# Performance work log

Hardware: AMD Instinct MI355X
Metric: run time of the kernel (lower is better)

The kernel has to match this reference:

```python
import jax, jax.numpy as jnp
import numpy as np

NUM_TREE = 64
TREE_DEPTH = 4
NUM_LEAF = 2 ** (TREE_DEPTH + 1)        # 32
NUM_INTERNALS = NUM_LEAF - 1            # 31
IN_DIM = 512
OUT_DIM = 16
BATCH = 8192


def build_route_masks(tree_depth: int, num_internals: int, num_leaf: int) -> np.ndarray:
    """Static gather indices into the [p, 1-p] concatenated prob vector (length 2*num_internals).
    Returns [tree_depth+1, num_leaf]; product over level axis gives leaf path probabilities.
    Mirrors the increment_mask construction in the torch forward."""
    masks = []
    num_repeat = num_leaf // 2
    num_local_internals = 1
    masks.append(np.repeat(np.array([0, num_internals]), num_repeat))
    for _ in range(1, tree_depth + 1):
        num_repeat //= 2
        num_local_internals *= 2
        m = np.repeat(np.arange(num_local_internals - 1, 2 * num_local_internals - 1), 2)
        m = m + np.tile(np.array([0, num_internals]), num_local_internals)
        m = np.repeat(m, num_repeat)
        masks.append(m)
    return np.stack(masks).astype(np.int32)  # [depth+1, num_leaf]


ROUTE_MASKS = jnp.asarray(build_route_masks(TREE_DEPTH, NUM_INTERNALS, NUM_LEAF))


def setup_inputs() -> dict:
    key = jax.random.key(0)
    k1, k2, k3 = jax.random.split(key, 3)
    x = jax.random.normal(k1, (BATCH, IN_DIM), dtype=jnp.float32)
    # xavier-ish scale so sigmoid gates are not saturated
    W = jax.random.normal(k2, (NUM_TREE * NUM_INTERNALS, IN_DIM), dtype=jnp.float32) / np.sqrt(IN_DIM)
    b = jnp.zeros((NUM_TREE * NUM_INTERNALS,), dtype=jnp.float32)
    leafs = jax.random.normal(k3, (NUM_TREE, NUM_LEAF, OUT_DIM), dtype=jnp.float32)
    return {"x": x, "W": W, "b": b, "leafs": leafs}


def reference(x, W, b, leafs) -> jnp.ndarray:
    B = x.shape[0]
    T, L, O = leafs.shape
    I = L - 1
    tree_net = x @ W.T + b                                  # [B, T*I]
    p = jax.nn.sigmoid(tree_net).reshape(B, T, I)           # split per tree
    flat = jnp.concatenate([p, 1.0 - p], axis=-1)           # [B, T, 2I]
    gathered = flat[:, :, ROUTE_MASKS]                      # [B, T, depth+1, L]
    routes = jnp.prod(gathered, axis=2)                     # [B, T, L] leaf path probs
    leafs_sm = jax.nn.softmax(leafs, axis=-1)
    features = routes.reshape(B, T * L)
    out = features @ leafs_sm.reshape(T * L, O) / T
    return out
```

## Files before the change

### kernel.cpp

```cpp
#include <hip/hip_runtime.h>

#define BATCH 8192
#define IN_DIM 512
#define NT 64
#define NI 31
#define NL 32
#define ODIM 16
#define NPAD (NT*NL)

typedef __attribute__((ext_vector_type(8))) short bf16x8;
typedef __attribute__((ext_vector_type(4))) float f32x4;

__device__ __forceinline__ unsigned short f2b(float f) {
  union { float f; unsigned int u; } v; v.f = f;
  unsigned int r = v.u + 0x7fffu + ((v.u >> 16) & 1u);
  return (unsigned short)(r >> 16);
}
__device__ __forceinline__ float b2f(unsigned short h) {
  union { unsigned int u; float f; } v; v.u = ((unsigned int)h) << 16;
  return v.f;
}

__global__ __launch_bounds__(256) void prep_kernel(
    const float* __restrict__ x, const float* __restrict__ W,
    const float* __restrict__ leafs,
    unsigned short* __restrict__ xb, unsigned short* __restrict__ wb,
    float* __restrict__ lsm, float* __restrict__ out)
{
  const int NXg = BATCH * (IN_DIM/8);
  const int NWg = NPAD  * (IN_DIM/8);
  const int NS  = NT*NL;
  const int NZ  = BATCH*ODIM/4;
  int gid = blockIdx.x*256 + threadIdx.x;
  if (gid < NXg) {
    int row = gid >> 6, k8 = gid & 63;
    int kt = k8 >> 2, g = k8 & 3;
    int gs = g ^ ((row >> 1) & 3);
    const float* s = x + (size_t)row*IN_DIM + kt*32 + gs*8;
    float4 v0 = ((const float4*)s)[0], v1 = ((const float4*)s)[1];
    ushort4 o0, o1;
    o0.x=f2b(v0.x); o0.y=f2b(v0.y); o0.z=f2b(v0.z); o0.w=f2b(v0.w);
    o1.x=f2b(v1.x); o1.y=f2b(v1.y); o1.z=f2b(v1.z); o1.w=f2b(v1.w);
    ((ushort4*)xb)[gid*2]   = o0;
    ((ushort4*)xb)[gid*2+1] = o1;
  } else if ((gid -= NXg) < NWg) {
    int row = gid >> 6, k8 = gid & 63;
    int t = row >> 5, i = row & 31;
    int kt = k8 >> 2, g = k8 & 3;
    int gs = g ^ ((row >> 1) & 3);
    ushort4 o0, o1;
    if (i == 31) { o0.x=o0.y=o0.z=o0.w=0; o1=o0; }
    else {
      const float* s = W + (size_t)(t*NI+i)*IN_DIM + kt*32 + gs*8;
      float4 v0 = ((const float4*)s)[0], v1 = ((const float4*)s)[1];
      o0.x=f2b(v0.x); o0.y=f2b(v0.y); o0.z=f2b(v0.z); o0.w=f2b(v0.w);
      o1.x=f2b(v1.x); o1.y=f2b(v1.y); o1.z=f2b(v1.z); o1.w=f2b(v1.w);
    }
    ((ushort4*)wb)[gid*2]   = o0;
    ((ushort4*)wb)[gid*2+1] = o1;
  } else if ((gid -= NWg) < NS) {
    const float* src = leafs + (size_t)gid*ODIM;
    float m = src[0];
    #pragma unroll
    for (int o=1;o<ODIM;++o) m = fmaxf(m, src[o]);
    float e[ODIM]; float s = 0.f;
    #pragma unroll
    for (int o=0;o<ODIM;++o) { e[o] = __expf(src[o]-m); s += e[o]; }
    float inv = 1.f/(s*(float)NT);
    #pragma unroll
    for (int o=0;o<ODIM;++o) lsm[(size_t)gid*ODIM+o] = e[o]*inv;
  } else if ((gid -= NS) < NZ) {
    float4 zero = {0.f,0.f,0.f,0.f};
    ((float4*)out)[gid] = zero;
  }
}

__device__ __forceinline__ void async16(const unsigned short* g, unsigned short* l) {
  __builtin_amdgcn_global_load_lds(
      (const __attribute__((address_space(1))) unsigned int*)g,
      (__attribute__((address_space(3))) unsigned int*)l,
      16, 0, 0);
}

#define STG 12288

__global__ __launch_bounds__(256, 2) void fused_kernel(
    const unsigned short* __restrict__ xb, const unsigned short* __restrict__ wb,
    const float* __restrict__ bias, const float* __restrict__ lsm,
    float* __restrict__ out)
{
  __shared__ __align__(16) unsigned short smem[36864];

  const int tid  = threadIdx.x;
  const int lane = tid & 63;
  const int wave = tid >> 6;
  const int wm = wave & 1, wn = wave >> 1;

  const int bid = blockIdx.x;
  const int m_t = (bid & 7)*4 + (bid >> 7);
  const int n_t = (bid >> 3) & 15;
  const int m0 = m_t * 256, n0 = n_t * 128;

  f32x4 acc[8][4];
  #pragma unroll
  for (int i=0;i<8;++i)
    #pragma unroll
    for (int j=0;j<4;++j) { f32x4 z = {0.f,0.f,0.f,0.f}; acc[i][j] = z; }

  const int srow = lane >> 2, scol = (lane & 3) * 8;
  const unsigned short* gaw = xb + (size_t)(m0 + wave*64 + srow)*IN_DIM + scol;
  const unsigned short* gbw = wb + (size_t)(n0 + wave*32 + srow)*IN_DIM + scol;

  const int l15 = lane & 15, quad = lane >> 4;
  const int cs   = (quad ^ ((l15 >> 1) & 3)) << 3;

  #pragma unroll
  for (int c=0;c<4;++c) async16(gaw + c*16*IN_DIM,      smem + wave*2048 + c*512);
  #pragma unroll
  for (int c=0;c<2;++c) async16(gbw + c*16*IN_DIM,      smem + 8192 + wave*1024 + c*512);
  #pragma unroll
  for (int c=0;c<4;++c) async16(gaw + 32 + c*16*IN_DIM, smem + STG + wave*2048 + c*512);
  #pragma unroll
  for (int c=0;c<2;++c) async16(gbw + 32 + c*16*IN_DIM, smem + STG + 8192 + wave*1024 + c*512);

  unsigned short* st0 = smem;
  unsigned short* st1 = smem + STG;
  unsigned short* st2 = smem + 2*STG;

  for (int kt = 0; kt < 15; ++kt) {
    asm volatile("s_waitcnt vmcnt(6)" ::: "memory");
    __builtin_amdgcn_s_barrier();
    if (kt < 14) {
      const int ko = (kt + 2) * 32;
      #pragma unroll
      for (int c=0;c<4;++c)
        async16(gaw + ko + c*16*IN_DIM, st2 + wave*2048 + c*512);
      #pragma unroll
      for (int c=0;c<2;++c)
        async16(gbw + ko + c*16*IN_DIM, st2 + 8192 + wave*1024 + c*512);
    }
    const unsigned short* As = st0;
    const unsigned short* Bs = st0 + 8192;
    bf16x8 af[8], bfr[4];
    #pragma unroll
    for (int mi=0;mi<8;++mi)
      af[mi] = *(const bf16x8*)(As + (wm*128 + mi*16 + l15)*32 + cs);
    #pragma unroll
    for (int ni=0;ni<4;++ni)
      bfr[ni] = *(const bf16x8*)(Bs + (wn*64 + ni*16 + l15)*32 + cs);
    __builtin_amdgcn_s_setprio(1);
    #pragma unroll
    for (int mi=0;mi<8;++mi)
      #pragma unroll
      for (int ni=0;ni<4;++ni)
        acc[mi][ni] = __builtin_amdgcn_mfma_f32_16x16x32_bf16(
            af[mi], bfr[ni], acc[mi][ni], 0, 0, 0);
    __builtin_amdgcn_s_setprio(0);
    unsigned short* t = st0; st0 = st1; st1 = st2; st2 = t;
  }
  asm volatile("s_waitcnt vmcnt(0)" ::: "memory");
  __builtin_amdgcn_s_barrier();
  {
    const unsigned short* As = st0;
    const unsigned short* Bs = st0 + 8192;
    bf16x8 af[8], bfr[4];
    #pragma unroll
    for (int mi=0;mi<8;++mi)
      af[mi] = *(const bf16x8*)(As + (wm*128 + mi*16 + l15)*32 + cs);
    #pragma unroll
    for (int ni=0;ni<4;++ni)
      bfr[ni] = *(const bf16x8*)(Bs + (wn*64 + ni*16 + l15)*32 + cs);
    __builtin_amdgcn_s_setprio(1);
    #pragma unroll
    for (int mi=0;mi<8;++mi)
      #pragma unroll
      for (int ni=0;ni<4;++ni)
        acc[mi][ni] = __builtin_amdgcn_mfma_f32_16x16x32_bf16(
            af[mi], bfr[ni], acc[mi][ni], 0, 0, 0);
    __builtin_amdgcn_s_setprio(0);
  }

  bf16x8 bleaf[4];
  {
    const int t0 = n_t * 4;
    #pragma unroll
    for (int s=0;s<4;++s) {
      union { bf16x8 v; unsigned short u[8]; } tmp;
      #pragma unroll
      for (int j=0;j<8;++j)
        tmp.u[j] = f2b(lsm[((size_t)(t0+s)*NL + quad*8 + j)*ODIM + l15]);
      bleaf[s] = tmp.v;
    }
  }

  __syncthreads();

  unsigned short* Pt = smem;
  #pragma unroll
  for (int ni=0;ni<4;++ni) {
    int cl = wn*64 + ni*16 + l15;
    int gcol = n0 + cl;
    int tt = gcol >> 5, ii = gcol & 31;
    float bv = (ii < NI) ? bias[tt*NI + ii] : 0.f;
    #pragma unroll
    for (int mi=0;mi<8;++mi) {
      int lrow = wm*128 + mi*16 + quad*4;
      #pragma unroll
      for (int r=0;r<4;++r) {
        float v = acc[mi][ni][r] + bv;
        Pt[(lrow + r)*132 + cl] = f2b(1.f/(1.f + __expf(-v)));
      }
    }
  }
  __syncthreads();

  const int row = tid;
  unsigned int rt[64];
  #pragma unroll
  for (int tl=0; tl<4; ++tl) {
    const short4* pr4 = (const short4*)(Pt + row*132 + tl*32);
    union { short4 v4[8]; unsigned short u[32]; } qb;
    #pragma unroll
    for (int c=0;c<8;++c) qb.v4[c] = pr4[c];
    float q[31];
    #pragma unroll
    for (int i=0;i<31;++i) q[i] = b2f(qb.u[i]);
    float v[32];
    v[0] = q[0]; v[1] = 1.f - q[0];
    #pragma unroll
    for (int d=1; d<=4; ++d) {
      const int s = 1 << d;
      #pragma unroll
      for (int j=s-1; j>=0; --j) {
        float pj = q[(s-1)+j];
        float base = v[j];
        v[2*j]   = base * pj;
        v[2*j+1] = base * (1.f - pj);
      }
    }
    #pragma unroll
    for (int k=0;k<16;++k)
      rt[tl*16+k] = (unsigned int)f2b(v[2*k]) | ((unsigned int)f2b(v[2*k+1]) << 16);
  }
  __syncthreads();

  unsigned int* Rt32 = (unsigned int*)smem;
  {
    uint4* dst = (uint4*)(Rt32 + row*68);
    #pragma unroll
    for (int c=0;c<16;++c) {
      uint4 w; w.x=rt[c*4]; w.y=rt[c*4+1]; w.z=rt[c*4+2]; w.w=rt[c*4+3];
      dst[c] = w;
    }
  }
  __syncthreads();

  const unsigned short* RtS = smem;
  #pragma unroll
  for (int mt=0; mt<4; ++mt) {
    const int mrow = (wave*4 + mt)*16;
    f32x4 a2 = {0.f,0.f,0.f,0.f};
    #pragma unroll
    for (int s=0;s<4;++s) {
      bf16x8 af2 = *(const bf16x8*)(RtS + (mrow + l15)*136 + s*32 + quad*8);
      a2 = __builtin_amdgcn_mfma_f32_16x16x32_bf16(af2, bleaf[s], a2, 0, 0, 0);
    }
    float* op = out + (size_t)(m0 + mrow + quad*4)*ODIM + l15;
    #pragma unroll
    for (int r=0;r<4;++r)
      atomicAdd(op + r*ODIM, a2[r]);
  }
}

extern "C" void kernel_launch(void* const* d_in, const int* in_sizes, int n_in,
                              void* d_out, int out_size, void* d_ws, size_t ws_size,
                              hipStream_t stream) {
  const float* x     = (const float*)d_in[0];
  const float* W     = (const float*)d_in[1];
  const float* b     = (const float*)d_in[2];
  const float* leafs = (const float*)d_in[3];
  float* out = (float*)d_out;

  char* ws = (char*)d_ws;
  unsigned short* xb  = (unsigned short*)ws;
  unsigned short* wb  = (unsigned short*)(ws + 8388608);
  float*          lsm = (float*)(ws + 10485760);

  const int total = BATCH*(IN_DIM/8) + NPAD*(IN_DIM/8) + NT*NL + BATCH*ODIM/4;
  prep_kernel<<<dim3((total + 255)/256), dim3(256), 0, stream>>>(
      x, W, leafs, xb, wb, lsm, out);
  fused_kernel<<<dim3(512), dim3(256), 0, stream>>>(
      xb, wb, b, lsm, out);
}
```

Measured before the change: 104.6 us.

## Fuse x bf16 conversion into GEMM kernel via register-staged loads

Removes the separate pass that converted x to a bf16 workspace. The GEMM kernel now loads fp32 x rows directly into registers, packs them to bf16 with v_cvt_pk_bf16_f32, and writes them swizzled into LDS. The pipeline changes from a 3-stage async ring to double buffering, with register prefetch for A. This drops a full read and write of x in the prep pass but doubles the global bytes the GEMM reads for A. It also adds VALU conversion work and a shallower pipeline inside the main loop.

```diff
diff --git a/kernel.cpp b/kernel.cpp
--- a/kernel.cpp
+++ b/kernel.cpp
@@ -20,30 +20,22 @@
   union { unsigned int u; float f; } v; v.u = ((unsigned int)h) << 16;
   return v.f;
 }
+__device__ __forceinline__ unsigned int cvtpk(float lo, float hi) {
+  unsigned int r;
+  asm("v_cvt_pk_bf16_f32 %0, %1, %2" : "=v"(r) : "v"(lo), "v"(hi));
+  return r;
+}
 
 __global__ __launch_bounds__(256) void prep_kernel(
-    const float* __restrict__ x, const float* __restrict__ W,
-    const float* __restrict__ leafs,
-    unsigned short* __restrict__ xb, unsigned short* __restrict__ wb,
-    float* __restrict__ lsm, float* __restrict__ out)
+    const float* __restrict__ W, const float* __restrict__ leafs,
+    unsigned short* __restrict__ wb, float* __restrict__ lsm,
+    float* __restrict__ out)
 {
-  const int NXg = BATCH * (IN_DIM/8);
-  const int NWg = NPAD  * (IN_DIM/8);
+  const int NWg = NPAD * (IN_DIM/8);
   const int NS  = NT*NL;
   const int NZ  = BATCH*ODIM/4;
   int gid = blockIdx.x*256 + threadIdx.x;
-  if (gid < NXg) {
-    int row = gid >> 6, k8 = gid & 63;
-    int kt = k8 >> 2, g = k8 & 3;
-    int gs = g ^ ((row >> 1) & 3);
-    const float* s = x + (size_t)row*IN_DIM + kt*32 + gs*8;
-    float4 v0 = ((const float4*)s)[0], v1 = ((const float4*)s)[1];
-    ushort4 o0, o1;
-    o0.x=f2b(v0.x); o0.y=f2b(v0.y); o0.z=f2b(v0.z); o0.w=f2b(v0.w);
-    o1.x=f2b(v1.x); o1.y=f2b(v1.y); o1.z=f2b(v1.z); o1.w=f2b(v1.w);
-    ((ushort4*)xb)[gid*2]   = o0;
-    ((ushort4*)xb)[gid*2+1] = o1;
-  } else if ((gid -= NXg) < NWg) {
+  if (gid < NWg) {
     int row = gid >> 6, k8 = gid & 63;
     int t = row >> 5, i = row & 31;
     int kt = k8 >> 2, g = k8 & 3;
@@ -82,14 +74,14 @@
       16, 0, 0);
 }
 
-#define STG 12288
+#define SSTG 12288
 
 __global__ __launch_bounds__(256, 2) void fused_kernel(
-    const unsigned short* __restrict__ xb, const unsigned short* __restrict__ wb,
+    const float* __restrict__ x, const unsigned short* __restrict__ wb,
     const float* __restrict__ bias, const float* __restrict__ lsm,
     float* __restrict__ out)
 {
-  __shared__ __align__(16) unsigned short smem[36864];
+  __shared__ __align__(16) unsigned short smem[34816];
 
   const int tid  = threadIdx.x;
   const int lane = tid & 63;
@@ -108,39 +100,48 @@
     for (int j=0;j<4;++j) { f32x4 z = {0.f,0.f,0.f,0.f}; acc[i][j] = z; }
 
   const int srow = lane >> 2, scol = (lane & 3) * 8;
-  const unsigned short* gaw = xb + (size_t)(m0 + wave*64 + srow)*IN_DIM + scol;
   const unsigned short* gbw = wb + (size_t)(n0 + wave*32 + srow)*IN_DIM + scol;
+
+  const float4* gx4 = (const float4*)(x + (size_t)(m0 + tid)*IN_DIM);
+  const int aswz = (tid >> 1) & 3;
 
   const int l15 = lane & 15, quad = lane >> 4;
   const int cs   = (quad ^ ((l15 >> 1) & 3)) << 3;
 
-  #pragma unroll
-  for (int c=0;c<4;++c) async16(gaw + c*16*IN_DIM,      smem + wave*2048 + c*512);
-  #pragma unroll
-  for (int c=0;c<2;++c) async16(gbw + c*16*IN_DIM,      smem + 8192 + wave*1024 + c*512);
-  #pragma unroll
-  for (int c=0;c<4;++c) async16(gaw + 32 + c*16*IN_DIM, smem + STG + wave*2048 + c*512);
-  #pragma unroll
-  for (int c=0;c<2;++c) async16(gbw + 32 + c*16*IN_DIM, smem + STG + 8192 + wave*1024 + c*512);
-
-  unsigned short* st0 = smem;
-  unsigned short* st1 = smem + STG;
-  unsigned short* st2 = smem + 2*STG;
+  float4 L[8];
+
+  #pragma unroll
+  for (int j=0;j<8;++j) L[j] = gx4[j];
+  {
+    unsigned short* Ad = smem + tid*32;
+    #pragma unroll
+    for (int gsrc=0; gsrc<4; ++gsrc) {
+      uint4 w;
+      w.x = cvtpk(L[2*gsrc].x, L[2*gsrc].y);
+      w.y = cvtpk(L[2*gsrc].z, L[2*gsrc].w);
+      w.z = cvtpk(L[2*gsrc+1].x, L[2*gsrc+1].y);
+      w.w = cvtpk(L[2*gsrc+1].z, L[2*gsrc+1].w);
+      *(uint4*)(Ad + (gsrc ^ aswz)*8) = w;
+    }
+  }
+  #pragma unroll
+  for (int c=0;c<2;++c) async16(gbw + c*16*IN_DIM, smem + 8192 + wave*1024 + c*512);
+  __builtin_amdgcn_sched_barrier(0);
+  #pragma unroll
+  for (int j=0;j<8;++j) L[j] = gx4[8 + j];
 
   for (int kt = 0; kt < 15; ++kt) {
-    asm volatile("s_waitcnt vmcnt(6)" ::: "memory");
+    unsigned short* stc = smem + (kt & 1) * SSTG;
+    unsigned short* stn = smem + ((kt + 1) & 1) * SSTG;
+    asm volatile("s_waitcnt vmcnt(8) lgkmcnt(0)" ::: "memory");
     __builtin_amdgcn_s_barrier();
-    if (kt < 14) {
-      const int ko = (kt + 2) * 32;
-      #pragma unroll
-      for (int c=0;c<4;++c)
-        async16(gaw + ko + c*16*IN_DIM, st2 + wave*2048 + c*512);
-      #pragma unroll
-      for (int c=0;c<2;++c)
-        async16(gbw + ko + c*16*IN_DIM, st2 + 8192 + wave*1024 + c*512);
-    }
-    const unsigned short* As = st0;
-    const unsigned short* Bs = st0 + 8192;
+    #pragma unroll
+    for (int c=0;c<2;++c)
+      async16(gbw + (kt+1)*32 + c*16*IN_DIM, stn + 8192 + wave*1024 + c*512);
+    __builtin_amdgcn_sched_barrier(0);
+
+    const unsigned short* As = stc;
+    const unsigned short* Bs = stc + 8192;
     bf16x8 af[8], bfr[4];
     #pragma unroll
     for (int mi=0;mi<8;++mi)
@@ -156,13 +157,29 @@
         acc[mi][ni] = __builtin_amdgcn_mfma_f32_16x16x32_bf16(
             af[mi], bfr[ni], acc[mi][ni], 0, 0, 0);
     __builtin_amdgcn_s_setprio(0);
-    unsigned short* t = st0; st0 = st1; st1 = st2; st2 = t;
-  }
-  asm volatile("s_waitcnt vmcnt(0)" ::: "memory");
+
+    {
+      unsigned short* Ad = stn + tid*32;
+      #pragma unroll
+      for (int gsrc=0; gsrc<4; ++gsrc) {
+        uint4 w;
+        w.x = cvtpk(L[2*gsrc].x, L[2*gsrc].y);
+        w.y = cvtpk(L[2*gsrc].z, L[2*gsrc].w);
+        w.z = cvtpk(L[2*gsrc+1].x, L[2*gsrc+1].y);
+        w.w = cvtpk(L[2*gsrc+1].z, L[2*gsrc+1].w);
+        *(uint4*)(Ad + (gsrc ^ aswz)*8) = w;
+      }
+    }
+    if (kt < 14) {
+      #pragma unroll
+      for (int j=0;j<8;++j) L[j] = gx4[(kt+2)*8 + j];
+    }
+  }
+  asm volatile("s_waitcnt vmcnt(0) lgkmcnt(0)" ::: "memory");
   __builtin_amdgcn_s_barrier();
   {
-    const unsigned short* As = st0;
-    const unsigned short* Bs = st0 + 8192;
+    const unsigned short* As = smem + SSTG;
+    const unsigned short* Bs = smem + SSTG + 8192;
     bf16x8 af[8], bfr[4];
     #pragma unroll
     for (int mi=0;mi<8;++mi)
@@ -282,13 +299,12 @@
   float* out = (float*)d_out;
 
   char* ws = (char*)d_ws;
-  unsigned short* xb  = (unsigned short*)ws;
-  unsigned short* wb  = (unsigned short*)(ws + 8388608);
-  float*          lsm = (float*)(ws + 10485760);
-
-  const int total = BATCH*(IN_DIM/8) + NPAD*(IN_DIM/8) + NT*NL + BATCH*ODIM/4;
+  unsigned short* wb  = (unsigned short*)ws;
+  float*          lsm = (float*)(ws + 2097152);
+
+  const int total = NPAD*(IN_DIM/8) + NT*NL + BATCH*ODIM/4;
   prep_kernel<<<dim3((total + 255)/256), dim3(256), 0, stream>>>(
-      x, W, leafs, xb, wb, lsm, out);
+      W, leafs, wb, lsm, out);
   fused_kernel<<<dim3(512), dim3(256), 0, stream>>>(
-      xb, wb, b, lsm, out);
-}
+      x, wb, b, lsm, out);
+}
```

Result: slower. 118.8 us (+13.6%).
